# Kernel optimization log

Measured on AMD Instinct MI355X. Metric: run time of the kernel, lower is better.

## Reference

```python
import jax, jax.numpy as jnp
import numpy as np
from jax import lax

B, S, D, H, O = 128, 256, 128, 512, 25
TEMP = 0.1


def _init(key, shape, scale):
    return jax.random.uniform(key, shape, jnp.float32, -scale, scale)


def setup_inputs() -> dict:
    key = jax.random.key(0)
    ks = jax.random.split(key, 24)
    sH = 1.0 / np.sqrt(H)
    s2H = 1.0 / np.sqrt(2 * H)
    sD = 1.0 / np.sqrt(D)
    inp = {
        "x": jax.random.normal(ks[0], (B, S, D), jnp.float32),
        "noise_u": jnp.clip(jax.random.uniform(ks[1], (S, B, 1), jnp.float32), 1e-6, 1 - 1e-6),
        # layer_cin: Linear(D, H)
        "w_cin": _init(ks[2], (D, H), sD), "b_cin": _init(ks[3], (H,), sD),
        # layer_c MLP: 2H->2H (x3, ReLU) -> 1
        "w1": _init(ks[4], (2 * H, 2 * H), s2H), "b1": _init(ks[5], (2 * H,), s2H),
        "w2": _init(ks[6], (2 * H, 2 * H), s2H), "b2": _init(ks[7], (2 * H,), s2H),
        "w3": _init(ks[8], (2 * H, 2 * H), s2H), "b3": _init(ks[9], (2 * H,), s2H),
        "w4": _init(ks[10], (2 * H, 1), s2H), "b4": _init(ks[11], (1,), s2H),
        # GRUCell(H, H): gates ordered (r, z, n)
        "w_ih": _init(ks[12], (H, 3 * H), sH), "b_ih": _init(ks[13], (3 * H,), sH),
        "w_hh": _init(ks[14], (H, 3 * H), sH), "b_hh": _init(ks[15], (3 * H,), sH),
        # output Linear(H, O)
        "w_out": _init(ks[16], (H, O), sH), "b_out": _init(ks[17], (O,), sH),
    }
    return inp


def _gru_cell(x, h, w_ih, b_ih, w_hh, b_hh):
    gx = x @ w_ih + b_ih  # [B, 3H]
    gh = h @ w_hh + b_hh
    xr, xz, xn = jnp.split(gx, 3, axis=-1)
    hr, hz, hn = jnp.split(gh, 3, axis=-1)
    r = jax.nn.sigmoid(xr + hr)
    z = jax.nn.sigmoid(xz + hz)
    n = jnp.tanh(xn + r * hn)
    return (1.0 - z) * n + z * h


def reference(x, noise_u, w_cin, b_cin, w1, b1, w2, b2, w3, b3, w4, b4,
              w_ih, b_ih, w_hh, b_hh, w_out, b_out):
    xs = jnp.transpose(x, (1, 0, 2))  # [S, B, D]

    def step(carry, inp):
        c, h, n = carry
        x_t, u = inp
        c_in = jnp.tanh(x_t @ w_cin + b_cin)  # [B, H]
        com = jnp.concatenate([c, c_in], axis=1)  # [B, 2H]
        z = jax.nn.relu(com @ w1 + b1)
        z = jax.nn.relu(z @ w2 + b2)
        z = jax.nn.relu(z @ w3 + b3)
        alpha_logit = z @ w4 + b4  # [B, 1]
        # RelaxedBernoulli(temp=0.1).sample(): sigmoid((logits + logistic noise)/T), detached
        logistic = jnp.log(u) - jnp.log1p(-u)
        alpha = lax.stop_gradient(jax.nn.sigmoid((alpha_logit + logistic) / TEMP))
        h_gru = _gru_cell(c, h, w_ih, b_ih, w_hh, b_hh)
        h_new = h * (1.0 - alpha) + alpha * h_gru
        new_n = n * (1.0 - alpha) + 1.0
        c_new = (c * n * (1.0 - alpha) + c_in) / new_n
        return (c_new, h_new, new_n), None

    c0 = jnp.zeros((B, H), x.dtype)
    h0 = jnp.zeros((B, H), x.dtype)
    n0 = jnp.zeros((B, 1), x.dtype)
    (c, h, n), _ = lax.scan(step, (c0, h0, n0), (xs, noise_u))
    h = _gru_cell(c, h, w_ih, b_ih, w_hh, b_hh)  # final post-loop GRU step
    return h @ w_out + b_out
```

## Files before the change

### kernel.cpp

```cpp
#include <hip/hip_runtime.h>
#include <math.h>

#define SLEN 256
#define BSZ  128
#define DIN  128
#define HSZ  512
#define HH2  1024
#define GG3  1536
#define OSZ  25

typedef _Float16 h8 __attribute__((ext_vector_type(8)));
typedef _Float16 h4v __attribute__((ext_vector_type(4)));
typedef float    f4 __attribute__((ext_vector_type(4)));

struct P_t {
  const float *x, *noise, *b_cin, *b1, *b2, *b3, *w4, *b4, *b_ih, *b_hh, *w_out, *b_out;
  _Float16 *WT1, *WT2, *WT3, *WTih, *WThh, *WTcin;
  _Float16 *FW1T, *FW1B, *FW2, *FW3, *FWih, *FWhh;
  _Float16 *CIN, *Z1, *Z2, *HGRU16;
  float *LOGI, *C1, *D1, *CIH3, *G3;
  float *A1, *AIH3, *AHH3, *HF, *HGRUF, *NF, *PART;
  int *CNT, *DEAD;
  float *out;
};

__device__ __forceinline__ f4 mfma16(h8 a, h8 b, f4 c) {
  return __builtin_amdgcn_mfma_f32_16x16x32_f16(a, b, c, 0, 0, 0);
}

__device__ __forceinline__ float ldc_f(const float* p) {
  return __hip_atomic_load(p, __ATOMIC_RELAXED, __HIP_MEMORY_SCOPE_AGENT);
}
__device__ __forceinline__ void stc_f(float* p, float v) {
  __hip_atomic_store(p, v, __ATOMIC_RELAXED, __HIP_MEMORY_SCOPE_AGENT);
}
__device__ __forceinline__ unsigned ldc_u(const unsigned* p) {
  return __hip_atomic_load(p, __ATOMIC_RELAXED, __HIP_MEMORY_SCOPE_AGENT);
}
__device__ __forceinline__ void stc_u(unsigned* p, unsigned v) {
  __hip_atomic_store(p, v, __ATOMIC_RELAXED, __HIP_MEMORY_SCOPE_AGENT);
}

__device__ __forceinline__ void rtbar(int* cnt, int target, int* dead) {
  asm volatile("s_waitcnt vmcnt(0)" ::: "memory");
  __syncthreads();
  if (threadIdx.x == 0) {
    __hip_atomic_fetch_add(cnt, 1, __ATOMIC_RELAXED, __HIP_MEMORY_SCOPE_AGENT);
    int tries = 0;
    while (__hip_atomic_load(cnt, __ATOMIC_RELAXED, __HIP_MEMORY_SCOPE_AGENT) < target) {
      if (((++tries) & 63) == 0) {
        if (tries > (1 << 16) ||
            __hip_atomic_load(dead, __ATOMIC_RELAXED, __HIP_MEMORY_SCOPE_AGENT)) {
          __hip_atomic_store(dead, 1, __ATOMIC_RELAXED, __HIP_MEMORY_SCOPE_AGENT);
          break;
        }
      }
      __builtin_amdgcn_s_sleep(2);
    }
  }
  __syncthreads();
}

__global__ __launch_bounds__(256) void transpose_cvt(const float* __restrict__ src,
    _Float16* __restrict__ dst, int K, int N) {
  __shared__ float tl[32][33];
  int nt = N >> 5;
  int bx = blockIdx.x % nt, by = blockIdx.x / nt;
  int n0 = bx << 5, k0 = by << 5;
  int tx = threadIdx.x & 31, ty = threadIdx.x >> 5;
#pragma unroll
  for (int i = 0; i < 4; ++i) {
    int r = ty + (i << 3);
    tl[r][tx] = src[(size_t)(k0 + r) * N + n0 + tx];
  }
  __syncthreads();
#pragma unroll
  for (int i = 0; i < 4; ++i) {
    int r = ty + (i << 3);
    dst[(size_t)(n0 + r) * K + k0 + tx] = (_Float16)tl[tx][r];
  }
}

__global__ __launch_bounds__(512) void fragpack2(const _Float16* __restrict__ src,
    _Float16* __restrict__ dst, int srcK, int kOff, int K) {
  int ct = blockIdx.x;
  int chunks = (K / 32) * 64;
  for (int idx = threadIdx.x; idx < chunks; idx += 512) {
    int i = idx >> 6, lane = idx & 63;
    int mlw = lane & 15, qw = lane >> 4;
    *(h8*)(dst + ((size_t)ct * (K / 32) + i) * 512 + (size_t)lane * 8) =
        *(const h8*)(src + ((size_t)ct * 16 + mlw) * srcK + kOff + i * 32 + qw * 8);
  }
}

__global__ __launch_bounds__(256) void cin_kernel(P_t P) {
  int tid = blockIdx.x * blockDim.x + threadIdx.x;
  if (tid < SLEN * BSZ) {
    float u = P.noise[tid];
    P.LOGI[tid] = logf(u) - log1pf(-u);
  }
  int gw = tid >> 6, lane = tid & 63;
  int nw = (gridDim.x * blockDim.x) >> 6;
  int ml = lane & 15, q = lane >> 4;
  const int MT = (SLEN * BSZ) / 16;
  for (int tt = gw; tt < MT * 8; tt += nw) {
    int mt = tt & (MT - 1), nt = tt / MT;
    int m0 = mt * 16, n0 = nt * 64;
    int m = m0 + ml, b = m & 127, s = m >> 7;
    const float* ap = P.x + ((size_t)b * SLEN + s) * DIN + q * 8;
    const _Float16* bp = P.WTcin + (size_t)(n0 + ml) * DIN + q * 8;
    f4 a0 = {0,0,0,0}, a1 = a0, a2 = a0, a3 = a0;
#pragma unroll
    for (int k = 0; k < DIN; k += 32) {
      f4 lo = *(const f4*)(ap + k);
      f4 hi = *(const f4*)(ap + k + 4);
      h8 av;
      av[0] = (_Float16)lo[0]; av[1] = (_Float16)lo[1];
      av[2] = (_Float16)lo[2]; av[3] = (_Float16)lo[3];
      av[4] = (_Float16)hi[0]; av[5] = (_Float16)hi[1];
      av[6] = (_Float16)hi[2]; av[7] = (_Float16)hi[3];
      a0 = mfma16(av, *(const h8*)(bp + k),            a0);
      a1 = mfma16(av, *(const h8*)(bp + 16*DIN + k),   a1);
      a2 = mfma16(av, *(const h8*)(bp + 32*DIN + k),   a2);
      a3 = mfma16(av, *(const h8*)(bp + 48*DIN + k),   a3);
    }
#pragma unroll
    for (int r = 0; r < 4; ++r) {
      int row = m0 + q * 4 + r;
      int c0 = n0 + ml;
      P.CIN[(size_t)row * HSZ + c0     ] = (_Float16)tanhf(a0[r] + P.b_cin[c0]);
      P.CIN[(size_t)row * HSZ + c0 + 16] = (_Float16)tanhf(a1[r] + P.b_cin[c0 + 16]);
      P.CIN[(size_t)row * HSZ + c0 + 32] = (_Float16)tanhf(a2[r] + P.b_cin[c0 + 32]);
      P.CIN[(size_t)row * HSZ + c0 + 48] = (_Float16)tanhf(a3[r] + P.b_cin[c0 + 48]);
    }
  }
}

__global__ __launch_bounds__(256) void init_kernel(P_t P) {
  int idx = blockIdx.x * 256 + threadIdx.x;
  for (int i = idx; i < BSZ * HH2; i += 65536) P.A1[i] = 0.f;
  for (int i = idx; i < BSZ * HSZ * 3; i += 65536) { P.AIH3[i] = 0.f; P.AHH3[i] = 0.f; }
  if (idx < BSZ * HSZ) P.HF[idx] = 0.f;
  if (idx < 2 * BSZ) P.NF[idx] = 0.f;
  if (idx < 128) P.CNT[idx] = 0;
  if (idx == 0) P.DEAD[0] = 0;
}

__global__ __launch_bounds__(256) void boot_kernel(P_t P) {
  const int tid = threadIdx.x, lane = tid & 63, wv = tid >> 6;
  const int ml = lane & 15, q = lane >> 4;
  const int g = blockIdx.x * 4 + wv;
  {
    int rt = g & 7, ct = g >> 3, m0 = rt << 4, col = (ct << 4) + ml;
    const _Float16* a0 = P.CIN + (size_t)(m0 + ml) * HSZ + q * 8;
    const _Float16* bp = P.FW1B + (size_t)ct * 16 * 512 + (size_t)lane * 8;
    f4 acc = {0.f, 0.f, 0.f, 0.f};
#pragma unroll
    for (int k = 0; k < 16; ++k)
      acc = mfma16(*(const h8*)(a0 + k * 32), *(const h8*)(bp + (size_t)k * 512), acc);
    float bia = P.b1[col];
#pragma unroll
    for (int j = 0; j < 4; ++j)
      P.Z1[(size_t)(m0 + q * 4 + j) * HH2 + col] = (_Float16)fmaxf(acc[j] + bia, 0.f);
  }
  int e = blockIdx.x * 512 + tid;
#pragma unroll
  for (int rep = 0; rep < 2; ++rep, e += 256) {
    int row = e >> 9, cc = e & 511;
    float rg = 1.f / (1.f + expf(-(P.b_ih[cc] + P.b_hh[cc])));
    float zg = 1.f / (1.f + expf(-(P.b_ih[cc + 512] + P.b_hh[cc + 512])));
    float ng = tanhf(P.b_ih[cc + 1024] + rg * P.b_hh[cc + 1024]);
    float v = (1.f - zg) * ng;
    P.HGRUF[(size_t)row * HSZ + cc] = v;
    P.HGRU16[(size_t)row * HSZ + cc] = (_Float16)v;
  }
}

__global__ __launch_bounds__(512, 2) void step_node(P_t P, int t) {
  const int tid = threadIdx.x;
  const int lane = tid & 63, wv = tid >> 6;
  const int ml = lane & 15, q = lane >> 4;
  const int b = blockIdx.x, rt = b >> 5, sub = b & 31;
  const int m0 = rt << 4;
  const int slot = sub * 8 + wv;
  __shared__ unsigned sZd[16 * 516];
  __shared__ float sAl[16], sNN[16];
  int* cnt  = P.CNT + rt * 16;
  int* dead = P.DEAD;

  if (sub < 8) {
    int ct = slot, col = (ct << 4) + ml;
    const _Float16* a0 = P.Z1 + (size_t)(m0 + ml) * HH2 + q * 8;
    const _Float16* bp = P.FW2 + (size_t)ct * 32 * 512 + (size_t)lane * 8;
    f4 acc = {0.f, 0.f, 0.f, 0.f};
#pragma unroll
    for (int k = 0; k < 32; ++k)
      acc = mfma16(*(const h8*)(a0 + k * 32), *(const h8*)(bp + (size_t)k * 512), acc);
    float bia = P.b2[col];
#pragma unroll
    for (int j = 0; j < 4; ++j) {
      _Float16 hv = (_Float16)fmaxf(acc[j] + bia, 0.f);
      unsigned short mb = __builtin_bit_cast(unsigned short, hv);
      unsigned ob = (unsigned)__shfl_xor((int)mb, 1) & 0xffffu;
      if (!(ml & 1))
        stc_u((unsigned*)&P.Z2[(size_t)(m0 + q * 4 + j) * HH2 + col],
              (unsigned)mb | (ob << 16));
    }
  } else {
    int ts = slot - 64;
    for (int e = ts; e < 320; e += 192) {
      f4 acc = {0.f, 0.f, 0.f, 0.f};
      if (e < 96) {
        int ct = e, col = (ct << 4) + ml;
        const _Float16* a0 = P.HGRU16 + (size_t)(m0 + ml) * HSZ + q * 8;
        const _Float16* bp = P.FWhh + (size_t)ct * 16 * 512 + (size_t)lane * 8;
#pragma unroll
        for (int k = 0; k < 16; ++k)
          acc = mfma16(*(const h8*)(a0 + k * 32), *(const h8*)(bp + (size_t)k * 512), acc);
        int gate = col >> 9, cc = col & 511;
#pragma unroll
        for (int j = 0; j < 4; ++j)
          stc_f(P.G3 + ((size_t)(m0 + q * 4 + j) * 512 + cc) * 3 + gate, acc[j]);
      } else if (e < 160) {
        int ct = e - 96, col = (ct << 4) + ml;
        const _Float16* a0 = P.CIN + ((size_t)t * BSZ + m0 + ml) * HSZ + q * 8;
        const _Float16* bp = P.FW1T + (size_t)ct * 16 * 512 + (size_t)lane * 8;
#pragma unroll
        for (int k = 0; k < 16; ++k)
          acc = mfma16(*(const h8*)(a0 + k * 32), *(const h8*)(bp + (size_t)k * 512), acc);
#pragma unroll
        for (int j = 0; j < 4; ++j)
          stc_f(P.C1 + (size_t)(m0 + q * 4 + j) * HH2 + col, acc[j]);
      } else if (e < 256) {
        int ct = e - 160, col = (ct << 4) + ml;
        const _Float16* a0 = P.CIN + ((size_t)t * BSZ + m0 + ml) * HSZ + q * 8;
        const _Float16* bp = P.FWih + (size_t)ct * 16 * 512 + (size_t)lane * 8;
#pragma unroll
        for (int k = 0; k < 16; ++k)
          acc = mfma16(*(const h8*)(a0 + k * 32), *(const h8*)(bp + (size_t)k * 512), acc);
        int gate = col >> 9, cc = col & 511;
#pragma unroll
        for (int j = 0; j < 4; ++j)
          stc_f(P.CIH3 + ((size_t)(m0 + q * 4 + j) * 512 + cc) * 3 + gate, acc[j]);
      } else if (t + 1 < SLEN) {
        int ct = e - 256, col = (ct << 4) + ml;
        const _Float16* a0 = P.CIN + ((size_t)(t + 1) * BSZ + m0 + ml) * HSZ + q * 8;
        const _Float16* bp = P.FW1B + (size_t)ct * 16 * 512 + (size_t)lane * 8;
#pragma unroll
        for (int k = 0; k < 16; ++k)
          acc = mfma16(*(const h8*)(a0 + k * 32), *(const h8*)(bp + (size_t)k * 512), acc);
#pragma unroll
        for (int j = 0; j < 4; ++j)
          stc_f(P.D1 + (size_t)(m0 + q * 4 + j) * HH2 + col, acc[j]);
      }
    }
  }
  rtbar(cnt, t * 64 + 32, dead);

  const int rA = tid >> 5, cA = (sub << 5) + (tid & 31);
  const size_t oA = (size_t)(m0 + rA) * HH2 + cA;
  float c1v = ldc_f(P.C1 + oA);
  float d1v = (t + 1 < SLEN) ? ldc_f(P.D1 + oA) : 0.f;
  float a1old = P.A1[oA];
  float b1v = P.b1[cA];
  const int r3 = tid >> 4, cc3 = (sub << 4) + (tid & 15);
  const size_t o3 = ((size_t)(m0 + r3) * 512 + cc3) * 3;
  const size_t oh = (size_t)(m0 + r3) * HSZ + cc3;
  float cih0 = 0, cih1 = 0, cih2 = 0, g0 = 0, g1 = 0, g2 = 0;
  float aih0 = 0, aih1 = 0, aih2 = 0, ahh0 = 0, ahh1 = 0, ahh2 = 0;
  float bi0 = 0, bi1 = 0, bi2 = 0, bh0 = 0, bh1 = 0, bh2 = 0;
  float hfold = 0, hgrold = 0;
  if (tid < 256) {
    cih0 = ldc_f(P.CIH3 + o3); cih1 = ldc_f(P.CIH3 + o3 + 1); cih2 = ldc_f(P.CIH3 + o3 + 2);
    g0 = ldc_f(P.G3 + o3); g1 = ldc_f(P.G3 + o3 + 1); g2 = ldc_f(P.G3 + o3 + 2);
    aih0 = P.AIH3[o3]; aih1 = P.AIH3[o3 + 1]; aih2 = P.AIH3[o3 + 2];
    ahh0 = P.AHH3[o3]; ahh1 = P.AHH3[o3 + 1]; ahh2 = P.AHH3[o3 + 2];
    bi0 = P.b_ih[cc3]; bi1 = P.b_ih[cc3 + 512]; bi2 = P.b_ih[cc3 + 1024];
    bh0 = P.b_hh[cc3]; bh1 = P.b_hh[cc3 + 512]; bh2 = P.b_hh[cc3 + 1024];
    hfold = P.HF[oh]; hgrold = P.HGRUF[oh];
  }
  if (sub < 8) {
    unsigned vb[16];
    const unsigned* z2d = (const unsigned*)P.Z2 + (size_t)m0 * 512;
#pragma unroll
    for (int j = 0; j < 16; ++j) vb[j] = ldc_u(z2d + (size_t)j * 512 + tid);
#pragma unroll
    for (int j = 0; j < 16; ++j) sZd[j * 516 + tid] = vb[j];
    __syncthreads();
    int ct = slot, col = (ct << 4) + ml;
    const _Float16* a0 = (const _Float16*)sZd + ml * 1032 + q * 8;
    const _Float16* bp = P.FW3 + (size_t)ct * 32 * 512 + (size_t)lane * 8;
    f4 acc = {0.f, 0.f, 0.f, 0.f};
#pragma unroll
    for (int k = 0; k < 32; ++k)
      acc = mfma16(*(const h8*)(a0 + k * 32), *(const h8*)(bp + (size_t)k * 512), acc);
    float bia = P.b3[col], w4v = P.w4[col];
#pragma unroll
    for (int j = 0; j < 4; ++j) {
      float v = fmaxf(acc[j] + bia, 0.f) * w4v;
      v += __shfl_xor(v, 1); v += __shfl_xor(v, 2);
      v += __shfl_xor(v, 4); v += __shfl_xor(v, 8);
      if (ml == 0) stc_f(P.PART + (size_t)ct * BSZ + m0 + q * 4 + j, v);
    }
  }
  rtbar(cnt, t * 64 + 64, dead);

  if (wv == 0) {
    int r = lane & 15, pq = lane >> 4;
    int row = m0 + r;
    float v = 0.f;
#pragma unroll
    for (int k = 0; k < 16; ++k)
      v += ldc_f(P.PART + (size_t)(pq * 16 + k) * BSZ + row);
    v += __shfl_xor(v, 16); v += __shfl_xor(v, 32);
    if (lane < 16) {
      float lg = (v + P.b4[0] + P.LOGI[(size_t)t * BSZ + row]) * 10.0f;
      float al = 1.f / (1.f + expf(-lg));
      float no = P.NF[((t + 1) & 1) * BSZ + row];
      float nn = no * (1.f - al) + 1.f;
      sAl[r] = al; sNN[r] = nn;
      if (sub == 0) P.NF[(t & 1) * BSZ + row] = nn;
    }
  }
  __syncthreads();
  {
    float al = sAl[rA], om = 1.f - al, rin = 1.f / sNN[rA];
    float a = om * a1old + c1v;
    P.A1[oA] = a;
    if (t + 1 < SLEN)
      P.Z1[oA] = (_Float16)fmaxf(a * rin + d1v + b1v, 0.f);
  }
  if (tid < 256) {
    float al = sAl[r3], om = 1.f - al, rin = 1.f / sNN[r3];
    float air = om * aih0 + cih0, aiz = om * aih1 + cih1, ain = om * aih2 + cih2;
    P.AIH3[o3] = air; P.AIH3[o3 + 1] = aiz; P.AIH3[o3 + 2] = ain;
    float ahr = om * ahh0 + al * g0, ahz = om * ahh1 + al * g1, ahn = om * ahh2 + al * g2;
    P.AHH3[o3] = ahr; P.AHH3[o3 + 1] = ahz; P.AHH3[o3 + 2] = ahn;
    float gxr = air * rin + bi0, gxz = aiz * rin + bi1, gxn = ain * rin + bi2;
    float ghr = ahr + bh0, ghz = ahz + bh1, ghn = ahn + bh2;
    float rg = 1.f / (1.f + expf(-(gxr + ghr)));
    float zg = 1.f / (1.f + expf(-(gxz + ghz)));
    float ng = tanhf(gxn + rg * ghn);
    float hnew = om * hfold + al * hgrold;
    P.HF[oh] = hnew;
    float hg1 = (1.f - zg) * ng + zg * hnew;
    P.HGRUF[oh] = hg1;
    P.HGRU16[oh] = (_Float16)hg1;
  }
}

__global__ __launch_bounds__(256) void final_out(P_t P) {
  __shared__ float hf[512];
  const int r = blockIdx.x, tid = threadIdx.x;
  const int lane = tid & 63, wv = tid >> 6;
  for (int e = tid; e < 512; e += 256) hf[e] = P.HGRUF[(size_t)r * HSZ + e];
  __syncthreads();
  for (int c = wv; c < OSZ; c += 4) {
    float v = 0.f;
#pragma unroll
    for (int j = 0; j < 8; ++j)
      v += hf[lane + 64 * j] * P.w_out[(size_t)(lane + 64 * j) * OSZ + c];
    for (int off = 32; off > 0; off >>= 1) v += __shfl_xor(v, off);
    if (lane == 0) P.out[r * OSZ + c] = v + P.b_out[c];
  }
}

extern "C" void kernel_launch(void* const* d_in, const int* in_sizes, int n_in,
                              void* d_out, int out_size, void* d_ws, size_t ws_size,
                              hipStream_t stream) {
  const float* x     = (const float*)d_in[0];
  const float* noise = (const float*)d_in[1];
  const float* w_cin = (const float*)d_in[2];
  const float* b_cin = (const float*)d_in[3];
  const float* w1    = (const float*)d_in[4];
  const float* b1    = (const float*)d_in[5];
  const float* w2    = (const float*)d_in[6];
  const float* b2    = (const float*)d_in[7];
  const float* w3    = (const float*)d_in[8];
  const float* b3    = (const float*)d_in[9];
  const float* w4    = (const float*)d_in[10];
  const float* b4    = (const float*)d_in[11];
  const float* w_ih  = (const float*)d_in[12];
  const float* b_ih  = (const float*)d_in[13];
  const float* w_hh  = (const float*)d_in[14];
  const float* b_hh  = (const float*)d_in[15];
  const float* w_out = (const float*)d_in[16];
  const float* b_out = (const float*)d_in[17];

  char* ws = (char*)d_ws;
  size_t off = 0;
  auto alloc = [&](size_t bytes) -> void* {
    void* p = ws + off;
    off = (off + bytes + 255) & ~(size_t)255;
    return p;
  };

  P_t P;
  P.x = x; P.noise = noise; P.b_cin = b_cin; P.b1 = b1; P.b2 = b2; P.b3 = b3;
  P.w4 = w4; P.b4 = b4; P.b_ih = b_ih; P.b_hh = b_hh; P.w_out = w_out; P.b_out = b_out;
  P.WT1    = (_Float16*)alloc((size_t)HH2 * HH2 * 2);
  P.WT2    = (_Float16*)alloc((size_t)HH2 * HH2 * 2);
  P.WT3    = (_Float16*)alloc((size_t)HH2 * HH2 * 2);
  P.WTih   = (_Float16*)alloc((size_t)GG3 * HSZ * 2);
  P.WThh   = (_Float16*)alloc((size_t)GG3 * HSZ * 2);
  P.WTcin  = (_Float16*)alloc((size_t)HSZ * DIN * 2);
  P.FW1T   = (_Float16*)alloc((size_t)HH2 * 512 * 2);
  P.FW1B   = (_Float16*)alloc((size_t)HH2 * 512 * 2);
  P.FW2    = (_Float16*)alloc((size_t)HH2 * HH2 * 2);
  P.FW3    = (_Float16*)alloc((size_t)HH2 * HH2 * 2);
  P.FWih   = (_Float16*)alloc((size_t)GG3 * HSZ * 2);
  P.FWhh   = (_Float16*)alloc((size_t)GG3 * HSZ * 2);
  P.CIN    = (_Float16*)alloc((size_t)SLEN * BSZ * HSZ * 2);
  P.Z1     = (_Float16*)alloc((size_t)BSZ * HH2 * 2);
  P.Z2     = (_Float16*)alloc((size_t)BSZ * HH2 * 2);
  P.HGRU16 = (_Float16*)alloc((size_t)BSZ * HSZ * 2);
  P.LOGI   = (float*)alloc((size_t)SLEN * BSZ * 4);
  P.C1     = (float*)alloc((size_t)BSZ * HH2 * 4);
  P.D1     = (float*)alloc((size_t)BSZ * HH2 * 4);
  P.CIH3   = (float*)alloc((size_t)BSZ * HSZ * 3 * 4);
  P.G3     = (float*)alloc((size_t)BSZ * HSZ * 3 * 4);
  P.A1     = (float*)alloc((size_t)BSZ * HH2 * 4);
  P.AIH3   = (float*)alloc((size_t)BSZ * HSZ * 3 * 4);
  P.AHH3   = (float*)alloc((size_t)BSZ * HSZ * 3 * 4);
  P.HF     = (float*)alloc((size_t)BSZ * HSZ * 4);
  P.HGRUF  = (float*)alloc((size_t)BSZ * HSZ * 4);
  P.NF     = (float*)alloc((size_t)2 * BSZ * 4);
  P.PART   = (float*)alloc((size_t)64 * BSZ * 4);
  P.CNT    = (int*)alloc(128 * 4);
  P.DEAD   = (int*)alloc(64 * 4);
  P.out    = (float*)d_out;

  transpose_cvt<<<(HH2/32)*(HH2/32), 256, 0, stream>>>(w1, P.WT1, HH2, HH2);
  transpose_cvt<<<(HH2/32)*(HH2/32), 256, 0, stream>>>(w2, P.WT2, HH2, HH2);
  transpose_cvt<<<(HH2/32)*(HH2/32), 256, 0, stream>>>(w3, P.WT3, HH2, HH2);
  transpose_cvt<<<(GG3/32)*(HSZ/32), 256, 0, stream>>>(w_ih, P.WTih, HSZ, GG3);
  transpose_cvt<<<(GG3/32)*(HSZ/32), 256, 0, stream>>>(w_hh, P.WThh, HSZ, GG3);
  transpose_cvt<<<(HSZ/32)*(DIN/32), 256, 0, stream>>>(w_cin, P.WTcin, DIN, HSZ);
  fragpack2<<<HH2/16, 512, 0, stream>>>(P.WT1, P.FW1T, HH2, 0, 512);
  fragpack2<<<HH2/16, 512, 0, stream>>>(P.WT1, P.FW1B, HH2, 512, 512);
  fragpack2<<<HH2/16, 512, 0, stream>>>(P.WT2, P.FW2, HH2, 0, HH2);
  fragpack2<<<HH2/16, 512, 0, stream>>>(P.WT3, P.FW3, HH2, 0, HH2);
  fragpack2<<<GG3/16, 512, 0, stream>>>(P.WTih, P.FWih, HSZ, 0, HSZ);
  fragpack2<<<GG3/16, 512, 0, stream>>>(P.WThh, P.FWhh, HSZ, 0, HSZ);

  cin_kernel<<<1024, 256, 0, stream>>>(P);
  init_kernel<<<256, 256, 0, stream>>>(P);
  boot_kernel<<<128, 256, 0, stream>>>(P);

  for (int t = 0; t < SLEN; ++t)
    step_node<<<256, 512, 0, stream>>>(P, t);
  final_out<<<BSZ, 256, 0, stream>>>(P);
}
```

Baseline: 7.281 ms.

## Split per-step kernel into two launches, replacing first grid barrier

Replaces the single per-timestep kernel, which used two software grid barriers, with two kernels per step. node_a computes the Z2, hidden-gate, C1, input-gate and D1 products across 768 single-wave blocks, each producing four 16-column tiles. node_b then runs the third MLP layer straight from global memory and keeps one barrier before the state update. This drops one spin barrier and the LDS staging, and uses plain stores instead of atomic stores. In exchange it adds 256 extra kernel launches and a round trip through global memory between the two kernels.

```diff
diff --git a/kernel.cpp b/kernel.cpp
--- a/kernel.cpp
+++ b/kernel.cpp
@@ -32,12 +32,6 @@
   return __hip_atomic_load(p, __ATOMIC_RELAXED, __HIP_MEMORY_SCOPE_AGENT);
 }
 __device__ __forceinline__ void stc_f(float* p, float v) {
-  __hip_atomic_store(p, v, __ATOMIC_RELAXED, __HIP_MEMORY_SCOPE_AGENT);
-}
-__device__ __forceinline__ unsigned ldc_u(const unsigned* p) {
-  return __hip_atomic_load(p, __ATOMIC_RELAXED, __HIP_MEMORY_SCOPE_AGENT);
-}
-__device__ __forceinline__ void stc_u(unsigned* p, unsigned v) {
   __hip_atomic_store(p, v, __ATOMIC_RELAXED, __HIP_MEMORY_SCOPE_AGENT);
 }
 
@@ -176,134 +170,174 @@
   }
 }
 
-__global__ __launch_bounds__(512, 2) void step_node(P_t P, int t) {
+__global__ __launch_bounds__(64) void node_a(P_t P, int t) {
+  const int lane = threadIdx.x;
+  const int ml = lane & 15, q = lane >> 4;
+  const int g = blockIdx.x;
+  f4 ac0 = {0.f,0.f,0.f,0.f}, ac1 = ac0, ac2 = ac0, ac3 = ac0;
+  if (g < 128) {
+    int rt = g & 7, c64 = g >> 3, m0 = rt << 4;
+    const _Float16* ap = P.Z1 + (size_t)(m0 + ml) * HH2 + q * 8;
+    const _Float16* bp = P.FW2 + (size_t)c64 * 4 * 16384 + (size_t)lane * 8;
+#pragma unroll
+    for (int k = 0; k < 32; ++k) {
+      h8 av = *(const h8*)(ap + k * 32);
+      ac0 = mfma16(av, *(const h8*)(bp + (size_t)k * 512        ), ac0);
+      ac1 = mfma16(av, *(const h8*)(bp + (size_t)k * 512 + 16384), ac1);
+      ac2 = mfma16(av, *(const h8*)(bp + (size_t)k * 512 + 32768), ac2);
+      ac3 = mfma16(av, *(const h8*)(bp + (size_t)k * 512 + 49152), ac3);
+    }
+    int cb = c64 * 64 + ml;
+    float b0 = P.b2[cb], b1 = P.b2[cb+16], b2 = P.b2[cb+32], b3 = P.b2[cb+48];
+#pragma unroll
+    for (int j = 0; j < 4; ++j) {
+      size_t ro = (size_t)(m0 + q*4 + j) * HH2 + cb;
+      P.Z2[ro     ] = (_Float16)fmaxf(ac0[j] + b0, 0.f);
+      P.Z2[ro + 16] = (_Float16)fmaxf(ac1[j] + b1, 0.f);
+      P.Z2[ro + 32] = (_Float16)fmaxf(ac2[j] + b2, 0.f);
+      P.Z2[ro + 48] = (_Float16)fmaxf(ac3[j] + b3, 0.f);
+    }
+  } else if (g < 320) {
+    int u = g - 128; int rt = u & 7, c64 = u >> 3, m0 = rt << 4;
+    const _Float16* ap = P.HGRU16 + (size_t)(m0 + ml) * HSZ + q * 8;
+    const _Float16* bp = P.FWhh + (size_t)c64 * 4 * 8192 + (size_t)lane * 8;
+#pragma unroll
+    for (int k = 0; k < 16; ++k) {
+      h8 av = *(const h8*)(ap + k * 32);
+      ac0 = mfma16(av, *(const h8*)(bp + (size_t)k * 512        ), ac0);
+      ac1 = mfma16(av, *(const h8*)(bp + (size_t)k * 512 +  8192), ac1);
+      ac2 = mfma16(av, *(const h8*)(bp + (size_t)k * 512 + 16384), ac2);
+      ac3 = mfma16(av, *(const h8*)(bp + (size_t)k * 512 + 24576), ac3);
+    }
+    int base = c64 * 64;
+#pragma unroll
+    for (int uu = 0; uu < 4; ++uu) {
+      f4 a = uu==0?ac0:uu==1?ac1:uu==2?ac2:ac3;
+      int colq = base + uu * 16;
+      int gate = colq >> 9, cc = (colq & 511) + ml;
+#pragma unroll
+      for (int j = 0; j < 4; ++j)
+        P.G3[((size_t)(m0 + q*4 + j) * 512 + cc) * 3 + gate] = a[j];
+    }
+  } else if (g < 448) {
+    int u = g - 320; int rt = u & 7, c64 = u >> 3, m0 = rt << 4;
+    const _Float16* ap = P.CIN + ((size_t)t * BSZ + m0 + ml) * HSZ + q * 8;
+    const _Float16* bp = P.FW1T + (size_t)c64 * 4 * 8192 + (size_t)lane * 8;
+#pragma unroll
+    for (int k = 0; k < 16; ++k) {
+      h8 av = *(const h8*)(ap + k * 32);
+      ac0 = mfma16(av, *(const h8*)(bp + (size_t)k * 512        ), ac0);
+      ac1 = mfma16(av, *(const h8*)(bp + (size_t)k * 512 +  8192), ac1);
+      ac2 = mfma16(av, *(const h8*)(bp + (size_t)k * 512 + 16384), ac2);
+      ac3 = mfma16(av, *(const h8*)(bp + (size_t)k * 512 + 24576), ac3);
+    }
+    int cb = c64 * 64 + ml;
+#pragma unroll
+    for (int j = 0; j < 4; ++j) {
+      size_t ro = (size_t)(m0 + q*4 + j) * HH2 + cb;
+      P.C1[ro] = ac0[j]; P.C1[ro+16] = ac1[j]; P.C1[ro+32] = ac2[j]; P.C1[ro+48] = ac3[j];
+    }
+  } else if (g < 640) {
+    int u = g - 448; int rt = u & 7, c64 = u >> 3, m0 = rt << 4;
+    const _Float16* ap = P.CIN + ((size_t)t * BSZ + m0 + ml) * HSZ + q * 8;
+    const _Float16* bp = P.FWih + (size_t)c64 * 4 * 8192 + (size_t)lane * 8;
+#pragma unroll
+    for (int k = 0; k < 16; ++k) {
+      h8 av = *(const h8*)(ap + k * 32);
+      ac0 = mfma16(av, *(const h8*)(bp + (size_t)k * 512        ), ac0);
+      ac1 = mfma16(av, *(const h8*)(bp + (size_t)k * 512 +  8192), ac1);
+      ac2 = mfma16(av, *(const h8*)(bp + (size_t)k * 512 + 16384), ac2);
+      ac3 = mfma16(av, *(const h8*)(bp + (size_t)k * 512 + 24576), ac3);
+    }
+    int base = c64 * 64;
+#pragma unroll
+    for (int uu = 0; uu < 4; ++uu) {
+      f4 a = uu==0?ac0:uu==1?ac1:uu==2?ac2:ac3;
+      int colq = base + uu * 16;
+      int gate = colq >> 9, cc = (colq & 511) + ml;
+#pragma unroll
+      for (int j = 0; j < 4; ++j)
+        P.CIH3[((size_t)(m0 + q*4 + j) * 512 + cc) * 3 + gate] = a[j];
+    }
+  } else {
+    if (t + 1 < SLEN) {
+      int u = g - 640; int rt = u & 7, c64 = u >> 3, m0 = rt << 4;
+      const _Float16* ap = P.CIN + ((size_t)(t + 1) * BSZ + m0 + ml) * HSZ + q * 8;
+      const _Float16* bp = P.FW1B + (size_t)c64 * 4 * 8192 + (size_t)lane * 8;
+#pragma unroll
+      for (int k = 0; k < 16; ++k) {
+        h8 av = *(const h8*)(ap + k * 32);
+        ac0 = mfma16(av, *(const h8*)(bp + (size_t)k * 512        ), ac0);
+        ac1 = mfma16(av, *(const h8*)(bp + (size_t)k * 512 +  8192), ac1);
+        ac2 = mfma16(av, *(const h8*)(bp + (size_t)k * 512 + 16384), ac2);
+        ac3 = mfma16(av, *(const h8*)(bp + (size_t)k * 512 + 24576), ac3);
+      }
+      int cb = c64 * 64 + ml;
+#pragma unroll
+      for (int j = 0; j < 4; ++j) {
+        size_t ro = (size_t)(m0 + q*4 + j) * HH2 + cb;
+        P.D1[ro] = ac0[j]; P.D1[ro+16] = ac1[j]; P.D1[ro+32] = ac2[j]; P.D1[ro+48] = ac3[j];
+      }
+    }
+  }
+}
+
+__global__ __launch_bounds__(256, 2) void node_b(P_t P, int t) {
   const int tid = threadIdx.x;
   const int lane = tid & 63, wv = tid >> 6;
   const int ml = lane & 15, q = lane >> 4;
   const int b = blockIdx.x, rt = b >> 5, sub = b & 31;
   const int m0 = rt << 4;
-  const int slot = sub * 8 + wv;
-  __shared__ unsigned sZd[16 * 516];
   __shared__ float sAl[16], sNN[16];
   int* cnt  = P.CNT + rt * 16;
   int* dead = P.DEAD;
 
-  if (sub < 8) {
-    int ct = slot, col = (ct << 4) + ml;
-    const _Float16* a0 = P.Z1 + (size_t)(m0 + ml) * HH2 + q * 8;
-    const _Float16* bp = P.FW2 + (size_t)ct * 32 * 512 + (size_t)lane * 8;
-    f4 acc = {0.f, 0.f, 0.f, 0.f};
-#pragma unroll
-    for (int k = 0; k < 32; ++k)
-      acc = mfma16(*(const h8*)(a0 + k * 32), *(const h8*)(bp + (size_t)k * 512), acc);
-    float bia = P.b2[col];
-#pragma unroll
-    for (int j = 0; j < 4; ++j) {
-      _Float16 hv = (_Float16)fmaxf(acc[j] + bia, 0.f);
-      unsigned short mb = __builtin_bit_cast(unsigned short, hv);
-      unsigned ob = (unsigned)__shfl_xor((int)mb, 1) & 0xffffu;
-      if (!(ml & 1))
-        stc_u((unsigned*)&P.Z2[(size_t)(m0 + q * 4 + j) * HH2 + col],
-              (unsigned)mb | (ob << 16));
-    }
-  } else {
-    int ts = slot - 64;
-    for (int e = ts; e < 320; e += 192) {
-      f4 acc = {0.f, 0.f, 0.f, 0.f};
-      if (e < 96) {
-        int ct = e, col = (ct << 4) + ml;
-        const _Float16* a0 = P.HGRU16 + (size_t)(m0 + ml) * HSZ + q * 8;
-        const _Float16* bp = P.FWhh + (size_t)ct * 16 * 512 + (size_t)lane * 8;
-#pragma unroll
-        for (int k = 0; k < 16; ++k)
-          acc = mfma16(*(const h8*)(a0 + k * 32), *(const h8*)(bp + (size_t)k * 512), acc);
-        int gate = col >> 9, cc = col & 511;
-#pragma unroll
-        for (int j = 0; j < 4; ++j)
-          stc_f(P.G3 + ((size_t)(m0 + q * 4 + j) * 512 + cc) * 3 + gate, acc[j]);
-      } else if (e < 160) {
-        int ct = e - 96, col = (ct << 4) + ml;
-        const _Float16* a0 = P.CIN + ((size_t)t * BSZ + m0 + ml) * HSZ + q * 8;
-        const _Float16* bp = P.FW1T + (size_t)ct * 16 * 512 + (size_t)lane * 8;
-#pragma unroll
-        for (int k = 0; k < 16; ++k)
-          acc = mfma16(*(const h8*)(a0 + k * 32), *(const h8*)(bp + (size_t)k * 512), acc);
-#pragma unroll
-        for (int j = 0; j < 4; ++j)
-          stc_f(P.C1 + (size_t)(m0 + q * 4 + j) * HH2 + col, acc[j]);
-      } else if (e < 256) {
-        int ct = e - 160, col = (ct << 4) + ml;
-        const _Float16* a0 = P.CIN + ((size_t)t * BSZ + m0 + ml) * HSZ + q * 8;
-        const _Float16* bp = P.FWih + (size_t)ct * 16 * 512 + (size_t)lane * 8;
-#pragma unroll
-        for (int k = 0; k < 16; ++k)
-          acc = mfma16(*(const h8*)(a0 + k * 32), *(const h8*)(bp + (size_t)k * 512), acc);
-        int gate = col >> 9, cc = col & 511;
-#pragma unroll
-        for (int j = 0; j < 4; ++j)
-          stc_f(P.CIH3 + ((size_t)(m0 + q * 4 + j) * 512 + cc) * 3 + gate, acc[j]);
-      } else if (t + 1 < SLEN) {
-        int ct = e - 256, col = (ct << 4) + ml;
-        const _Float16* a0 = P.CIN + ((size_t)(t + 1) * BSZ + m0 + ml) * HSZ + q * 8;
-        const _Float16* bp = P.FW1B + (size_t)ct * 16 * 512 + (size_t)lane * 8;
-#pragma unroll
-        for (int k = 0; k < 16; ++k)
-          acc = mfma16(*(const h8*)(a0 + k * 32), *(const h8*)(bp + (size_t)k * 512), acc);
-#pragma unroll
-        for (int j = 0; j < 4; ++j)
-          stc_f(P.D1 + (size_t)(m0 + q * 4 + j) * HH2 + col, acc[j]);
-      }
-    }
-  }
-  rtbar(cnt, t * 64 + 32, dead);
-
-  const int rA = tid >> 5, cA = (sub << 5) + (tid & 31);
-  const size_t oA = (size_t)(m0 + rA) * HH2 + cA;
-  float c1v = ldc_f(P.C1 + oA);
-  float d1v = (t + 1 < SLEN) ? ldc_f(P.D1 + oA) : 0.f;
-  float a1old = P.A1[oA];
+  const int rA = tid >> 5;
+  const int cA = (sub << 5) + (tid & 31);
+  const size_t oA0 = (size_t)(m0 + rA) * HH2 + cA;
+  const size_t oA1 = (size_t)(m0 + rA + 8) * HH2 + cA;
+  float a1o0 = P.A1[oA0], c1v0 = P.C1[oA0];
+  float a1o1 = P.A1[oA1], c1v1 = P.C1[oA1];
+  float d1v0 = 0.f, d1v1 = 0.f;
+  if (t + 1 < SLEN) { d1v0 = P.D1[oA0]; d1v1 = P.D1[oA1]; }
   float b1v = P.b1[cA];
   const int r3 = tid >> 4, cc3 = (sub << 4) + (tid & 15);
   const size_t o3 = ((size_t)(m0 + r3) * 512 + cc3) * 3;
   const size_t oh = (size_t)(m0 + r3) * HSZ + cc3;
-  float cih0 = 0, cih1 = 0, cih2 = 0, g0 = 0, g1 = 0, g2 = 0;
-  float aih0 = 0, aih1 = 0, aih2 = 0, ahh0 = 0, ahh1 = 0, ahh2 = 0;
-  float bi0 = 0, bi1 = 0, bi2 = 0, bh0 = 0, bh1 = 0, bh2 = 0;
-  float hfold = 0, hgrold = 0;
-  if (tid < 256) {
-    cih0 = ldc_f(P.CIH3 + o3); cih1 = ldc_f(P.CIH3 + o3 + 1); cih2 = ldc_f(P.CIH3 + o3 + 2);
-    g0 = ldc_f(P.G3 + o3); g1 = ldc_f(P.G3 + o3 + 1); g2 = ldc_f(P.G3 + o3 + 2);
-    aih0 = P.AIH3[o3]; aih1 = P.AIH3[o3 + 1]; aih2 = P.AIH3[o3 + 2];
-    ahh0 = P.AHH3[o3]; ahh1 = P.AHH3[o3 + 1]; ahh2 = P.AHH3[o3 + 2];
-    bi0 = P.b_ih[cc3]; bi1 = P.b_ih[cc3 + 512]; bi2 = P.b_ih[cc3 + 1024];
-    bh0 = P.b_hh[cc3]; bh1 = P.b_hh[cc3 + 512]; bh2 = P.b_hh[cc3 + 1024];
-    hfold = P.HF[oh]; hgrold = P.HGRUF[oh];
-  }
+  float cih0 = P.CIH3[o3], cih1 = P.CIH3[o3 + 1], cih2 = P.CIH3[o3 + 2];
+  float g0 = P.G3[o3], g1 = P.G3[o3 + 1], g2 = P.G3[o3 + 2];
+  float aih0 = P.AIH3[o3], aih1 = P.AIH3[o3 + 1], aih2 = P.AIH3[o3 + 2];
+  float ahh0 = P.AHH3[o3], ahh1 = P.AHH3[o3 + 1], ahh2 = P.AHH3[o3 + 2];
+  float bi0 = P.b_ih[cc3], bi1 = P.b_ih[cc3 + 512], bi2 = P.b_ih[cc3 + 1024];
+  float bh0 = P.b_hh[cc3], bh1 = P.b_hh[cc3 + 512], bh2 = P.b_hh[cc3 + 1024];
+  float hfold = P.HF[oh], hgrold = P.HGRUF[oh];
+
   if (sub < 8) {
-    unsigned vb[16];
-    const unsigned* z2d = (const unsigned*)P.Z2 + (size_t)m0 * 512;
-#pragma unroll
-    for (int j = 0; j < 16; ++j) vb[j] = ldc_u(z2d + (size_t)j * 512 + tid);
-#pragma unroll
-    for (int j = 0; j < 16; ++j) sZd[j * 516 + tid] = vb[j];
-    __syncthreads();
-    int ct = slot, col = (ct << 4) + ml;
-    const _Float16* a0 = (const _Float16*)sZd + ml * 1032 + q * 8;
-    const _Float16* bp = P.FW3 + (size_t)ct * 32 * 512 + (size_t)lane * 8;
-    f4 acc = {0.f, 0.f, 0.f, 0.f};
-#pragma unroll
-    for (int k = 0; k < 32; ++k)
-      acc = mfma16(*(const h8*)(a0 + k * 32), *(const h8*)(bp + (size_t)k * 512), acc);
-    float bia = P.b3[col], w4v = P.w4[col];
-#pragma unroll
-    for (int j = 0; j < 4; ++j) {
-      float v = fmaxf(acc[j] + bia, 0.f) * w4v;
-      v += __shfl_xor(v, 1); v += __shfl_xor(v, 2);
-      v += __shfl_xor(v, 4); v += __shfl_xor(v, 8);
-      if (ml == 0) stc_f(P.PART + (size_t)ct * BSZ + m0 + q * 4 + j, v);
-    }
-  }
-  rtbar(cnt, t * 64 + 64, dead);
+    int c32 = sub * 4 + wv;
+    const _Float16* ap = P.Z2 + (size_t)(m0 + ml) * HH2 + q * 8;
+    const _Float16* bp = P.FW3 + (size_t)c32 * 2 * 16384 + (size_t)lane * 8;
+    f4 ac0 = {0.f,0.f,0.f,0.f}, ac1 = ac0;
+#pragma unroll
+    for (int k = 0; k < 32; ++k) {
+      h8 av = *(const h8*)(ap + k * 32);
+      ac0 = mfma16(av, *(const h8*)(bp + (size_t)k * 512        ), ac0);
+      ac1 = mfma16(av, *(const h8*)(bp + (size_t)k * 512 + 16384), ac1);
+    }
+#pragma unroll
+    for (int uu = 0; uu < 2; ++uu) {
+      f4 a = uu ? ac1 : ac0;
+      int ct = c32 * 2 + uu, col = (ct << 4) + ml;
+      float bia = P.b3[col], w4v = P.w4[col];
+#pragma unroll
+      for (int j = 0; j < 4; ++j) {
+        float v = fmaxf(a[j] + bia, 0.f) * w4v;
+        v += __shfl_xor(v, 1); v += __shfl_xor(v, 2);
+        v += __shfl_xor(v, 4); v += __shfl_xor(v, 8);
+        if (ml == 0) stc_f(P.PART + (size_t)ct * BSZ + m0 + q * 4 + j, v);
+      }
+    }
+  }
+  rtbar(cnt, 32 * (t + 1), dead);
 
   if (wv == 0) {
     int r = lane & 15, pq = lane >> 4;
@@ -323,14 +357,21 @@
     }
   }
   __syncthreads();
+
   {
-    float al = sAl[rA], om = 1.f - al, rin = 1.f / sNN[rA];
-    float a = om * a1old + c1v;
-    P.A1[oA] = a;
+    float al0 = sAl[rA], om0 = 1.f - al0, ri0 = 1.f / sNN[rA];
+    float a = om0 * a1o0 + c1v0;
+    P.A1[oA0] = a;
     if (t + 1 < SLEN)
-      P.Z1[oA] = (_Float16)fmaxf(a * rin + d1v + b1v, 0.f);
-  }
-  if (tid < 256) {
+      P.Z1[oA0] = (_Float16)fmaxf(a * ri0 + d1v0 + b1v, 0.f);
+    float al1 = sAl[rA + 8], om1 = 1.f - al1, ri1 = 1.f / sNN[rA + 8];
+    float a2 = om1 * a1o1 + c1v1;
+    P.A1[oA1] = a2;
+    if (t + 1 < SLEN)
+      P.Z1[oA1] = (_Float16)fmaxf(a2 * ri1 + d1v1 + b1v, 0.f);
+  }
+
+  {
     float al = sAl[r3], om = 1.f - al, rin = 1.f / sNN[r3];
     float air = om * aih0 + cih0, aiz = om * aih1 + cih1, ain = om * aih2 + cih2;
     P.AIH3[o3] = air; P.AIH3[o3 + 1] = aiz; P.AIH3[o3 + 2] = ain;
@@ -447,7 +488,9 @@
   init_kernel<<<256, 256, 0, stream>>>(P);
   boot_kernel<<<128, 256, 0, stream>>>(P);
 
-  for (int t = 0; t < SLEN; ++t)
-    step_node<<<256, 512, 0, stream>>>(P, t);
+  for (int t = 0; t < SLEN; ++t) {
+    node_a<<<768, 64, 0, stream>>>(P, t);
+    node_b<<<256, 256, 0, stream>>>(P, t);
+  }
   final_out<<<BSZ, 256, 0, stream>>>(P);
 }
```

Measured after the change: 7.117 ms. -2.3%, faster.
